# Kernel optimization log

Measured on AMD Instinct MI355X. Metric: run time of the kernel, lower is better.

## Reference

```python
import jax, jax.numpy as jnp
import numpy as np

BLK = 32
BIT = 8
BN_EPS = 1e-5


def _ste(x, xq):
    # straight-through estimator: forward = xq, backward = identity
    return x + jax.lax.stop_gradient(xq - x)


def bfp_quant_act(x, bit=BIT, blk=BLK):
    # Block floating point: shared exponent over blocks of `blk` channels
    # at each (n, h, w); mantissa quantized to `bit` bits (incl. sign).
    N, C, H, W = x.shape
    xb = x.reshape(N, C // blk, blk, H, W)
    maxabs = jnp.max(jnp.abs(xb), axis=2, keepdims=True)
    e = jnp.floor(jnp.log2(jnp.maximum(maxabs, 1e-12)))  # shared exponent
    scale = jnp.exp2(e + 1.0 - (bit - 1))
    qmax = 2.0 ** (bit - 1)
    q = jnp.clip(jnp.round(xb / scale), -qmax, qmax - 1.0)
    xq = (q * scale).reshape(N, C, H, W)
    return _ste(x, xq)


def dsconv_weight_quant(w, bit=BIT, blk=BLK):
    # DSConv VQK: per-block (blk input channels, per output channel, per
    # spatial tap) integer quantization with a float per-block scale (KDS).
    O, I, kh, kw = w.shape
    wb = w.reshape(O, I // blk, blk, kh, kw)
    qmax = 2.0 ** (bit - 1) - 1.0
    scale = jnp.maximum(jnp.max(jnp.abs(wb), axis=2, keepdims=True), 1e-12) / qmax
    q = jnp.clip(jnp.round(wb / scale), -qmax - 1.0, qmax)
    wq = (q * scale).reshape(O, I, kh, kw)
    return _ste(w, wq)


def conv2d(x, w, stride, padding):
    return jax.lax.conv_general_dilated(
        x, w, window_strides=(stride, stride),
        padding=[(padding, padding), (padding, padding)],
        dimension_numbers=('NCHW', 'OIHW', 'NCHW'))


def batchnorm(x, g, b, m, v):
    inv = g / jnp.sqrt(v + BN_EPS)
    return x * inv[None, :, None, None] + (b - m * inv)[None, :, None, None]


def setup_inputs() -> dict:
    key = jax.random.key(0)
    ks = jax.random.split(key, 12)
    N, Cin, Cout, H, W = 64, 128, 256, 56, 56
    inp = {
        'x':  jax.random.normal(ks[0], (N, Cin, H, W), jnp.float32),
        'w1': jax.random.normal(ks[1], (Cout, Cin, 3, 3), jnp.float32) * 0.05,
        'w2': jax.random.normal(ks[2], (Cout, Cout, 3, 3), jnp.float32) * 0.05,
        'ws': jax.random.normal(ks[3], (Cout, Cin, 1, 1), jnp.float32) * 0.05,
        'bn1_g': jnp.ones((Cout,), jnp.float32),
        'bn1_b': jnp.zeros((Cout,), jnp.float32),
        'bn1_m': jax.random.normal(ks[4], (Cout,), jnp.float32) * 0.1,
        'bn1_v': jax.random.uniform(ks[5], (Cout,), jnp.float32, 0.5, 1.5),
        'bn2_g': jnp.ones((Cout,), jnp.float32),
        'bn2_b': jnp.zeros((Cout,), jnp.float32),
        'bn2_m': jax.random.normal(ks[6], (Cout,), jnp.float32) * 0.1,
        'bn2_v': jax.random.uniform(ks[7], (Cout,), jnp.float32, 0.5, 1.5),
        'bns_g': jnp.ones((Cout,), jnp.float32),
        'bns_b': jnp.zeros((Cout,), jnp.float32),
        'bns_m': jax.random.normal(ks[8], (Cout,), jnp.float32) * 0.1,
        'bns_v': jax.random.uniform(ks[9], (Cout,), jnp.float32, 0.5, 1.5),
    }
    return inp


def reference(x, w1, w2, ws, bn1_g, bn1_b, bn1_m, bn1_v,
              bn2_g, bn2_b, bn2_m, bn2_v, bns_g, bns_b, bns_m, bns_v):
    stride = 2
    # conv1 (DSConv 3x3, stride 2) -> BN -> ReLU -> BFP activation quant
    out = conv2d(x, dsconv_weight_quant(w1), stride, 1)
    out = jax.nn.relu(batchnorm(out, bn1_g, bn1_b, bn1_m, bn1_v))
    out = bfp_quant_act(out)
    # conv2 (DSConv 3x3, stride 1) -> BN
    out = conv2d(out, dsconv_weight_quant(w2), 1, 1)
    out = batchnorm(out, bn2_g, bn2_b, bn2_m, bn2_v)
    # downsample shortcut: DSConv 1x1 stride 2 -> BN
    sc = conv2d(x, dsconv_weight_quant(ws), stride, 0)
    sc = batchnorm(sc, bns_g, bns_b, bns_m, bns_v)
    out = jax.nn.relu(out + sc)
    out = bfp_quant_act(out)  # activation2 (last=False)
    return out
```

## Files before the change

### kernel.cpp

```cpp
#include <hip/hip_runtime.h>
#include <stdint.h>

typedef unsigned short u16;
typedef __bf16 bf16x8 __attribute__((ext_vector_type(8)));
typedef float f32x4 __attribute__((ext_vector_type(4)));

#define NB    64
#define CIN   128
#define COUT  256
#define PIMG  960
#define PTOT  61440

static constexpr size_t XT4_BYTES = (size_t)64*PTOT*8*2;
static constexpr size_t A1C_BYTES = (size_t)32*PTOT*8*2;
static constexpr size_t BT1_BYTES = (size_t)2*144*128*8*2;
static constexpr size_t BT2_BYTES = (size_t)2*304*128*8*2;
static constexpr size_t OFF_XT4  = 0;
static constexpr size_t OFF_A1C  = OFF_XT4 + XT4_BYTES;
static constexpr size_t OFF_B1   = OFF_A1C + A1C_BYTES;
static constexpr size_t OFF_B2   = OFF_B1 + BT1_BYTES;
static constexpr size_t OFF_BETA = OFF_B2 + BT2_BYTES;

static __device__ __forceinline__ u16 f2bf(float f) {
  uint32_t u = __float_as_uint(f);
  u += 0x7fffu + ((u >> 16) & 1u);
  return (u16)(u >> 16);
}

typedef const __attribute__((address_space(1))) uint32_t* gas1;
typedef __attribute__((address_space(3))) uint32_t* las3;
static __device__ __forceinline__ void gl16(const void* g, void* l) {
  __builtin_amdgcn_global_load_lds((gas1)(uintptr_t)g,
                                   (las3)(uint32_t)(uintptr_t)l, 16, 0, 0);
}

static __device__ __forceinline__ void quant2(float v0, float v1, float& o0, float& o1) {
  float mx = fmaxf(v0, v1);
  mx = fmaxf(mx, __shfl_xor(mx, 1));
  mx = fmaxf(mx, __shfl_xor(mx, 2));
  mx = fmaxf(mx, __shfl_xor(mx, 4));
  mx = fmaxf(mx, __shfl_xor(mx, 8));
  mx = fmaxf(mx, 1e-12f);
  const int e = (int)(__float_as_uint(mx) >> 23) - 127;
  const float scale = __uint_as_float((uint32_t)(e + 121) << 23);
  const float invs  = __uint_as_float((uint32_t)(133 - e) << 23);
  o0 = fminf(rintf(v0 * invs), 127.f) * scale;
  o1 = fminf(rintf(v1 * invs), 127.f) * scale;
}

__global__ void k_transpose(const float* __restrict__ x, u16* __restrict__ xt4) {
  __shared__ float s[32][33];
  const int ht = blockIdx.x, ct = blockIdx.y, n = blockIdx.z;
  const int t = threadIdx.x, tc = t >> 5, tw = t & 31;
  const float* src = x + ((size_t)(n*CIN + ct*32))*3136 + ht*32;
#pragma unroll
  for (int i = 0; i < 4; ++i)
    s[tc + i*8][tw] = src[(size_t)(tc + i*8)*3136 + tw];
  __syncthreads();
  const int c = ct*32 + tw;
#pragma unroll
  for (int i = 0; i < 4; ++i) {
    const int hwl = tc + i*8;
    const int hw = ht*32 + hwl;
    const int h = hw / 56, w = hw % 56;
    const int py = h + 1, px = w + 1;
    const int sub = (py & 1)*2 + (px & 1);
    const int p = (py >> 1)*32 + (px >> 1);
    xt4[(((size_t)(sub*16 + (c >> 3))*64 + n)*PIMG + p)*8 + (c & 7)]
        = f2bf(s[tw][hwl]);
  }
}

__global__ void k_prep(const float* __restrict__ w1, const float* __restrict__ w2,
                       const float* __restrict__ wsc,
                       const float* __restrict__ g1, const float* __restrict__ b1,
                       const float* __restrict__ m1, const float* __restrict__ v1,
                       const float* __restrict__ g2, const float* __restrict__ b2,
                       const float* __restrict__ m2, const float* __restrict__ v2,
                       const float* __restrict__ gs, const float* __restrict__ bs,
                       const float* __restrict__ ms, const float* __restrict__ vs,
                       u16* __restrict__ B1, u16* __restrict__ B2,
                       float* __restrict__ beta)
{
  const int id = blockIdx.x*256 + threadIdx.x;
  if (id < 9216) {
    const int o = id / 36, rem = id % 36, ib = rem / 9, t = rem % 9;
    const float inv = g1[o] / sqrtf(v1[o] + 1e-5f);
    const float* base = w1 + (size_t)(o*CIN + ib*32)*9 + t;
    float mx = 0.f;
#pragma unroll 8
    for (int jj = 0; jj < 32; ++jj) mx = fmaxf(mx, fabsf(base[jj*9]));
    const float scale = fmaxf(mx, 1e-12f) / 127.0f;
#pragma unroll 8
    for (int jj = 0; jj < 32; ++jj) {
      float q = rintf(base[jj*9] / scale);
      q = fminf(fmaxf(q, -128.f), 127.f);
      const int kc = t*16 + ib*4 + (jj >> 3);
      B1[(((size_t)(o >> 7)*144 + kc)*128 + (o & 127))*8 + (jj & 7)]
          = f2bf(q * scale * inv);
    }
  } else if (id < 27648) {
    const int id2 = id - 9216;
    const int o = id2 / 72, rem = id2 % 72, ib = rem / 9, t = rem % 9;
    const float inv = g2[o] / sqrtf(v2[o] + 1e-5f);
    const float* base = w2 + (size_t)(o*COUT + ib*32)*9 + t;
    float mx = 0.f;
#pragma unroll 8
    for (int jj = 0; jj < 32; ++jj) mx = fmaxf(mx, fabsf(base[jj*9]));
    const float scale = fmaxf(mx, 1e-12f) / 127.0f;
#pragma unroll 8
    for (int jj = 0; jj < 32; ++jj) {
      float q = rintf(base[jj*9] / scale);
      q = fminf(fmaxf(q, -128.f), 127.f);
      const int kc = t*32 + ib*4 + (jj >> 3);
      B2[(((size_t)(o >> 7)*304 + kc)*128 + (o & 127))*8 + (jj & 7)]
          = f2bf(q * scale * inv);
    }
  } else if (id < 28672) {
    const int id3 = id - 27648;
    const int o = id3 >> 2, ib = id3 & 3;
    const float inv = gs[o] / sqrtf(vs[o] + 1e-5f);
    const float* base = wsc + (size_t)o*CIN + ib*32;
    float mx = 0.f;
#pragma unroll 8
    for (int jj = 0; jj < 32; ++jj) mx = fmaxf(mx, fabsf(base[jj]));
    const float scale = fmaxf(mx, 1e-12f) / 127.0f;
#pragma unroll 8
    for (int jj = 0; jj < 32; ++jj) {
      float q = rintf(base[jj] / scale);
      q = fminf(fmaxf(q, -128.f), 127.f);
      const int kc = 288 + ib*4 + (jj >> 3);
      B2[(((size_t)(o >> 7)*304 + kc)*128 + (o & 127))*8 + (jj & 7)]
          = f2bf(q * scale * inv);
    }
  } else if (id < 29184) {
    const int id4 = id - 28672;
    const int which = id4 >> 8, o = id4 & 255;
    if (which == 0) {
      beta[o] = b1[o] - m1[o] * (g1[o] / sqrtf(v1[o] + 1e-5f));
    } else {
      beta[256 + o] = (b2[o] - m2[o] * (g2[o] / sqrtf(v2[o] + 1e-5f)))
                    + (bs[o] - ms[o] * (gs[o] / sqrtf(vs[o] + 1e-5f)));
    }
  }
}

template<int MODE>
__global__ __launch_bounds__(256, 2)
void gemm_k(const u16* __restrict__ Ag, const u16* __restrict__ Ag2,
            const u16* __restrict__ Bg, const float* __restrict__ beta,
            u16* __restrict__ a1c, float* __restrict__ of32)
{
  __shared__ __align__(16) u16 As[2][4][256][8];
  __shared__ __align__(16) u16 Bs[2][4][128][8];

  const int tid = threadIdx.x;
  const int wv  = tid >> 6;
  const int ln  = tid & 63;
  const int b   = blockIdx.x;
  const int xcd = b & 7, j = b >> 3;
  const int mtile = xcd*30 + (j % 30);
  const int ntile = j / 30;

  constexpr int NKA = (MODE == 0) ? 36 : 72;
  constexpr int NK  = (MODE == 0) ? 36 : 76;
  constexpr int NKC = (MODE == 0) ? 144 : 304;
  constexpr int GSH = (MODE == 0) ? 4 : 5;

  const int gp0 = mtile * 256;

  const char* const Bb = (const char*)Bg + (size_t)ntile*NKC*2048 + (size_t)ln*16;

  auto issue = [&](int nk, int slot) {
    const int kc = nk*4 + wv;
    const char* a;
    if (MODE == 1 && nk >= NKA) {
      const int g = kc - 288;
      a = (const char*)Ag2 + ((size_t)(48 + g)*PTOT + gp0)*16;
    } else if (MODE == 0) {
      const int t = kc >> GSH, g = kc & ((1 << GSH) - 1);
      const int dy = t / 3, dx = t - dy*3;
      const int sub = (dy & 1)*2 + (dx & 1);
      a = (const char*)Ag +
          ((size_t)(sub*16 + g)*PTOT + gp0 + (dy >> 1)*32 + (dx >> 1))*16;
    } else {
      const int t = kc >> GSH, g = kc & ((1 << GSH) - 1);
      const int dy = t / 3, dx = t - dy*3;
      a = (const char*)Ag + ((size_t)g*PTOT + gp0 + dy*32 + dx)*16;
    }
    a += (size_t)ln*16;
    const char* bb = Bb + (size_t)kc*2048;
    char* la = (char*)&As[slot][wv][0][0];
    char* lb = (char*)&Bs[slot][wv][0][0];
    gl16(a,        la);
    gl16(a + 1024, la + 1024);
    gl16(a + 2048, la + 2048);
    gl16(a + 3072, la + 3072);
    gl16(bb,        lb);
    gl16(bb + 1024, lb + 1024);
  };

  const int quad = ln >> 4, l15 = ln & 15;
  const int m_off = (wv & 1)*128, n_off = (wv >> 1)*64;
  const u16* ra[8];
  const u16* rb[4];
#pragma unroll
  for (int i = 0; i < 8; ++i)
    ra[i] = As[0][quad][m_off + i*16 + l15];
#pragma unroll
  for (int i = 0; i < 4; ++i)
    rb[i] = Bs[0][quad][n_off + i*16 + l15];

  f32x4 acc[8][4];
#pragma unroll
  for (int i = 0; i < 8; ++i)
#pragma unroll
    for (int j2 = 0; j2 < 4; ++j2)
      acc[i][j2] = (f32x4){0.f, 0.f, 0.f, 0.f};

  issue(0, 0);
  issue(1, 1);

  int buf = 0;
  for (int i = 0; i < NK; ++i) {
    if (i + 1 < NK)      asm volatile("s_waitcnt vmcnt(6)" ::: "memory");
    else                 asm volatile("s_waitcnt vmcnt(0)" ::: "memory");
    asm volatile("s_barrier" ::: "memory");

    const int aoff = buf * 8192;
    const int boff = buf * 4096;
    bf16x8 av[8], bv[4];
#pragma unroll
    for (int k = 0; k < 8; ++k) av[k] = *(const bf16x8*)(ra[k] + aoff);
#pragma unroll
    for (int k = 0; k < 4; ++k) bv[k] = *(const bf16x8*)(rb[k] + boff);
#pragma unroll
    for (int mi = 0; mi < 8; ++mi)
#pragma unroll
      for (int ni = 0; ni < 4; ++ni)
        acc[mi][ni] = __builtin_amdgcn_mfma_f32_16x16x32_bf16(av[mi], bv[ni], acc[mi][ni], 0, 0, 0);

    if (i + 2 < NK) {
      asm volatile("s_waitcnt lgkmcnt(0)" ::: "memory");
      asm volatile("s_barrier" ::: "memory");
      issue(i + 2, buf);
    }
    buf ^= 1;
  }

  const int cbase = ntile*128 + n_off;
  float bt[4];
#pragma unroll
  for (int ni = 0; ni < 4; ++ni) bt[ni] = beta[cbase + ni*16 + l15];

  const int gpw = gp0 + m_off;
  const int n0  = gpw / 960;
  const int r0  = gpw % 960;

  if constexpr (MODE == 0) {
#pragma unroll
    for (int mi = 0; mi < 8; ++mi)
#pragma unroll
      for (int r = 0; r < 4; ++r) {
        const int lo  = r0 + mi*16 + quad*4 + r;
        const int loc = (lo >= 960) ? lo - 960 : lo;
        if (loc < 896 && (loc & 31) < 28) {
          const int gp = gpw + mi*16 + quad*4 + r;
          float v[4];
#pragma unroll
          for (int ni = 0; ni < 4; ++ni) v[ni] = fmaxf(acc[mi][ni][r] + bt[ni], 0.f);
#pragma unroll
          for (int g = 0; g < 2; ++g) {
            float o0, o1;
            quant2(v[2*g], v[2*g+1], o0, o1);
            const int c0 = cbase + (2*g)*16 + l15;
            const int c1 = c0 + 16;
            a1c[((size_t)(c0 >> 3)*PTOT + gp + 33)*8 + (c0 & 7)]
                = (u16)(__float_as_uint(o0) >> 16);
            a1c[((size_t)(c1 >> 3)*PTOT + gp + 33)*8 + (c1 & 7)]
                = (u16)(__float_as_uint(o1) >> 16);
          }
        }
      }
  } else {
#pragma unroll
    for (int mi = 0; mi < 8; ++mi) {
      float ov[4][4];
#pragma unroll
      for (int r = 0; r < 4; ++r) {
        float v[4];
#pragma unroll
        for (int ni = 0; ni < 4; ++ni)
          v[ni] = fmaxf(acc[mi][ni][r] + bt[ni], 0.f);
#pragma unroll
        for (int g = 0; g < 2; ++g)
          quant2(v[2*g], v[2*g+1], ov[2*g][r], ov[2*g+1][r]);
      }
      const int lo   = r0 + mi*16 + quad*4;
      const int nimg = (lo >= 960) ? n0 + 1 : n0;
      const int loc  = (lo >= 960) ? lo - 960 : lo;
      const int x0 = loc & 31, y = loc >> 5;
      if (x0 < 28 && loc < 896) {
#pragma unroll
        for (int ni = 0; ni < 4; ++ni) {
          const int c = cbase + ni*16 + l15;
          f32x4 val = { ov[ni][0], ov[ni][1], ov[ni][2], ov[ni][3] };
          *(f32x4*)(of32 + ((size_t)(nimg*COUT + c)*28 + y)*28 + x0) = val;
        }
      }
    }
  }
}

extern "C" void kernel_launch(void* const* d_in, const int* in_sizes, int n_in,
                              void* d_out, int out_size, void* d_ws, size_t ws_size,
                              hipStream_t stream)
{
  (void)in_sizes; (void)n_in; (void)out_size; (void)ws_size;
  const float* x   = (const float*)d_in[0];
  const float* w1  = (const float*)d_in[1];
  const float* w2  = (const float*)d_in[2];
  const float* wsc = (const float*)d_in[3];
  const float* g1 = (const float*)d_in[4];
  const float* b1 = (const float*)d_in[5];
  const float* m1 = (const float*)d_in[6];
  const float* v1 = (const float*)d_in[7];
  const float* g2 = (const float*)d_in[8];
  const float* b2 = (const float*)d_in[9];
  const float* m2 = (const float*)d_in[10];
  const float* v2 = (const float*)d_in[11];
  const float* gs = (const float*)d_in[12];
  const float* bs = (const float*)d_in[13];
  const float* ms = (const float*)d_in[14];
  const float* vs = (const float*)d_in[15];

  char* ws = (char*)d_ws;
  u16* xt4  = (u16*)(ws + OFF_XT4);
  u16* a1c  = (u16*)(ws + OFF_A1C);
  u16* B1   = (u16*)(ws + OFF_B1);
  u16* B2   = (u16*)(ws + OFF_B2);
  float* beta = (float*)(ws + OFF_BETA);

  hipMemsetAsync(ws, 0, OFF_B1, stream);

  k_transpose<<<dim3(98, 4, 64), 256, 0, stream>>>(x, xt4);
  k_prep<<<114, 256, 0, stream>>>(w1, w2, wsc, g1, b1, m1, v1,
                                  g2, b2, m2, v2, gs, bs, ms, vs,
                                  B1, B2, beta);
  gemm_k<0><<<480, 256, 0, stream>>>(xt4, nullptr, B1, beta, a1c, nullptr);
  gemm_k<1><<<480, 256, 0, stream>>>(a1c, xt4, B2, beta + 256, nullptr, (float*)d_out);
}
```

Measured before the change: 355.0 us.

## Widen GEMM block to full N tile with triple-buffered A and interleaved prefetch

Each GEMM block now covers all 256 output channels with 8 waves (512 threads) instead of 128 channels with 4 waves, so every A tile is loaded from global memory once rather than twice and the grid halves. A uses a 3-stage LDS ring and B a 2-stage ring, each step consumes 8 k-chunks, and the A prefetch is split into four pieces interleaved with the MFMA phases, with setprio raised around the MFMAs. The goal is to cut redundant A traffic and hide load latency behind compute. In exchange LDS use and register pressure per block go up, which may limit occupancy, and 240 blocks could leave some CUs idle.

```diff
diff --git a/kernel.cpp b/kernel.cpp
--- a/kernel.cpp
+++ b/kernel.cpp
@@ -146,70 +146,69 @@
 }
 
 template<int MODE>
-__global__ __launch_bounds__(256, 2)
+__global__ __launch_bounds__(512, 2)
 void gemm_k(const u16* __restrict__ Ag, const u16* __restrict__ Ag2,
             const u16* __restrict__ Bg, const float* __restrict__ beta,
             u16* __restrict__ a1c, float* __restrict__ of32)
 {
-  __shared__ __align__(16) u16 As[2][4][256][8];
-  __shared__ __align__(16) u16 Bs[2][4][128][8];
+  __shared__ __align__(16) u16 As3[3][8][256][8];
+  __shared__ __align__(16) u16 Bs2[2][8][2][128][8];
 
   const int tid = threadIdx.x;
   const int wv  = tid >> 6;
   const int ln  = tid & 63;
-  const int b   = blockIdx.x;
-  const int xcd = b & 7, j = b >> 3;
-  const int mtile = xcd*30 + (j % 30);
-  const int ntile = j / 30;
-
-  constexpr int NKA = (MODE == 0) ? 36 : 72;
-  constexpr int NK  = (MODE == 0) ? 36 : 76;
+  const int wr  = wv >> 2;
+  const int wc  = wv & 3;
+
+  const int b = blockIdx.x;
+  const int mtile = (b & 7)*30 + (b >> 3);
+  const int gp0 = mtile * 256;
+
+  constexpr int NT  = (MODE == 0) ? 18 : 38;
   constexpr int NKC = (MODE == 0) ? 144 : 304;
-  constexpr int GSH = (MODE == 0) ? 4 : 5;
-
-  const int gp0 = mtile * 256;
-
-  const char* const Bb = (const char*)Bg + (size_t)ntile*NKC*2048 + (size_t)ln*16;
-
-  auto issue = [&](int nk, int slot) {
-    const int kc = nk*4 + wv;
-    const char* a;
-    if (MODE == 1 && nk >= NKA) {
+
+  auto a_src = [&](int kc) -> const char* {
+    if (MODE == 1 && kc >= 288) {
       const int g = kc - 288;
-      a = (const char*)Ag2 + ((size_t)(48 + g)*PTOT + gp0)*16;
+      return (const char*)Ag2 + ((size_t)(48 + g)*PTOT + gp0)*16;
     } else if (MODE == 0) {
-      const int t = kc >> GSH, g = kc & ((1 << GSH) - 1);
-      const int dy = t / 3, dx = t - dy*3;
+      const int t = kc >> 4, g = kc & 15;
+      const int dy = t/3, dx = t - dy*3;
       const int sub = (dy & 1)*2 + (dx & 1);
-      a = (const char*)Ag +
-          ((size_t)(sub*16 + g)*PTOT + gp0 + (dy >> 1)*32 + (dx >> 1))*16;
+      return (const char*)Ag +
+             ((size_t)(sub*16 + g)*PTOT + gp0 + (dy >> 1)*32 + (dx >> 1))*16;
     } else {
-      const int t = kc >> GSH, g = kc & ((1 << GSH) - 1);
-      const int dy = t / 3, dx = t - dy*3;
-      a = (const char*)Ag + ((size_t)g*PTOT + gp0 + dy*32 + dx)*16;
-    }
-    a += (size_t)ln*16;
-    const char* bb = Bb + (size_t)kc*2048;
-    char* la = (char*)&As[slot][wv][0][0];
-    char* lb = (char*)&Bs[slot][wv][0][0];
-    gl16(a,        la);
-    gl16(a + 1024, la + 1024);
-    gl16(a + 2048, la + 2048);
-    gl16(a + 3072, la + 3072);
-    gl16(bb,        lb);
-    gl16(bb + 1024, lb + 1024);
+      const int t = kc >> 5, g = kc & 31;
+      const int dy = t/3, dx = t - dy*3;
+      return (const char*)Ag + ((size_t)g*PTOT + gp0 + dy*32 + dx)*16;
+    }
   };
 
+  auto issueA4 = [&](int kt2, int slot) {
+    const char* s = a_src(kt2*8 + wv) + (size_t)ln*16;
+    char* d = (char*)&As3[slot][wv][0][0];
+#pragma unroll
+    for (int q = 0; q < 4; ++q) gl16(s + q*1024, d + q*1024);
+  };
+  auto issueB4 = [&](int kt2, int slot) {
+    const int kc = kt2*8 + wv;
+    const char* s0 = (const char*)Bg + (size_t)kc*2048 + (size_t)ln*16;
+    const char* s1 = s0 + (size_t)NKC*2048;
+    char* d = (char*)&Bs2[slot][wv][0][0][0];
+    gl16(s0,        d);
+    gl16(s0 + 1024, d + 1024);
+    gl16(s1,        d + 2048);
+    gl16(s1 + 1024, d + 3072);
+  };
+
   const int quad = ln >> 4, l15 = ln & 15;
-  const int m_off = (wv & 1)*128, n_off = (wv >> 1)*64;
-  const u16* ra[8];
-  const u16* rb[4];
-#pragma unroll
-  for (int i = 0; i < 8; ++i)
-    ra[i] = As[0][quad][m_off + i*16 + l15];
-#pragma unroll
-  for (int i = 0; i < 4; ++i)
-    rb[i] = Bs[0][quad][n_off + i*16 + l15];
+  const u16* aP = &As3[0][quad][wr*128 + l15][0];
+  const u16* bP[4];
+#pragma unroll
+  for (int ni = 0; ni < 4; ++ni) {
+    const int n_ = wc*64 + ni*16 + l15;
+    bP[ni] = &Bs2[0][quad][n_ >> 7][n_ & 127][0];
+  }
 
   f32x4 acc[8][4];
 #pragma unroll
@@ -218,42 +217,68 @@
     for (int j2 = 0; j2 < 4; ++j2)
       acc[i][j2] = (f32x4){0.f, 0.f, 0.f, 0.f};
 
-  issue(0, 0);
-  issue(1, 1);
-
-  int buf = 0;
-  for (int i = 0; i < NK; ++i) {
-    if (i + 1 < NK)      asm volatile("s_waitcnt vmcnt(6)" ::: "memory");
-    else                 asm volatile("s_waitcnt vmcnt(0)" ::: "memory");
+  issueA4(0, 0); issueB4(0, 0);
+  issueA4(1, 1); issueB4(1, 1);
+
+  int sl = 0;
+  for (int kt = 0; kt < NT; ++kt) {
+    const int bsl = kt & 1;
+    if (kt + 1 < NT) asm volatile("s_waitcnt vmcnt(8)" ::: "memory");
+    else             asm volatile("s_waitcnt vmcnt(0)" ::: "memory");
     asm volatile("s_barrier" ::: "memory");
 
-    const int aoff = buf * 8192;
-    const int boff = buf * 4096;
-    bf16x8 av[8], bv[4];
-#pragma unroll
-    for (int k = 0; k < 8; ++k) av[k] = *(const bf16x8*)(ra[k] + aoff);
-#pragma unroll
-    for (int k = 0; k < 4; ++k) bv[k] = *(const bf16x8*)(rb[k] + boff);
-#pragma unroll
-    for (int mi = 0; mi < 8; ++mi)
-#pragma unroll
-      for (int ni = 0; ni < 4; ++ni)
-        acc[mi][ni] = __builtin_amdgcn_mfma_f32_16x16x32_bf16(av[mi], bv[ni], acc[mi][ni], 0, 0, 0);
-
-    if (i + 2 < NK) {
+    bf16x8 bv[4][2];
+#pragma unroll
+    for (int ni = 0; ni < 4; ++ni)
+#pragma unroll
+      for (int ks = 0; ks < 2; ++ks)
+        bv[ni][ks] = *(const bf16x8*)(bP[ni] + bsl*16384 + ks*8192);
+
+    const u16* aB = aP + sl*16384;
+    const bool pre = (kt + 2 < NT);
+    int s2 = sl + 2; if (s2 >= 3) s2 -= 3;
+    const char* asrc = nullptr; char* adst = nullptr;
+    if (pre) {
+      asrc = a_src((kt + 2)*8 + wv) + (size_t)ln*16;
+      adst = (char*)&As3[s2][wv][0][0];
+    }
+
+#pragma unroll
+    for (int ph = 0; ph < 4; ++ph) {
+      bf16x8 av[2][2];
+#pragma unroll
+      for (int q = 0; q < 2; ++q)
+#pragma unroll
+        for (int ks = 0; ks < 2; ++ks)
+          av[q][ks] = *(const bf16x8*)(aB + ks*8192 + (ph*2 + q)*128);
+      if (pre) gl16(asrc + ph*1024, adst + ph*1024);
       asm volatile("s_waitcnt lgkmcnt(0)" ::: "memory");
-      asm volatile("s_barrier" ::: "memory");
-      issue(i + 2, buf);
-    }
-    buf ^= 1;
-  }
-
-  const int cbase = ntile*128 + n_off;
+      __builtin_amdgcn_sched_barrier(0);
+      if (ph == 3) {
+        asm volatile("s_barrier" ::: "memory");
+        if (pre) issueB4(kt + 2, bsl);
+      }
+      __builtin_amdgcn_s_setprio(1);
+#pragma unroll
+      for (int q = 0; q < 2; ++q) {
+        const int mi = ph*2 + q;
+#pragma unroll
+        for (int ni = 0; ni < 4; ++ni) {
+          acc[mi][ni] = __builtin_amdgcn_mfma_f32_16x16x32_bf16(av[q][0], bv[ni][0], acc[mi][ni], 0, 0, 0);
+          acc[mi][ni] = __builtin_amdgcn_mfma_f32_16x16x32_bf16(av[q][1], bv[ni][1], acc[mi][ni], 0, 0, 0);
+        }
+      }
+      __builtin_amdgcn_s_setprio(0);
+    }
+    sl = (sl == 2) ? 0 : sl + 1;
+  }
+
+  const int cbase = wc*64;
   float bt[4];
 #pragma unroll
   for (int ni = 0; ni < 4; ++ni) bt[ni] = beta[cbase + ni*16 + l15];
 
-  const int gpw = gp0 + m_off;
+  const int gpw = gp0 + wr*128;
   const int n0  = gpw / 960;
   const int r0  = gpw % 960;
 
@@ -347,6 +372,6 @@
   k_prep<<<114, 256, 0, stream>>>(w1, w2, wsc, g1, b1, m1, v1,
                                   g2, b2, m2, v2, gs, bs, ms, vs,
                                   B1, B2, beta);
-  gemm_k<0><<<480, 256, 0, stream>>>(xt4, nullptr, B1, beta, a1c, nullptr);
-  gemm_k<1><<<480, 256, 0, stream>>>(a1c, xt4, B2, beta + 256, nullptr, (float*)d_out);
-}
+  gemm_k<0><<<240, 512, 0, stream>>>(xt4, nullptr, B1, beta, a1c, nullptr);
+  gemm_k<1><<<240, 512, 0, stream>>>(a1c, xt4, B2, beta + 256, nullptr, (float*)d_out);
+}
```

Result: faster. 346.0 us (-2.5%).
